# Performance work log

Measured on AMD Instinct MI355X. Metric: run time of the kernel, lower is better.

Reference implementation:

```python
import jax, jax.numpy as jnp
import numpy as np

N_NODES = 100000
N_EDGES = 1000000
NUM_FEATURES = 64
HIDDEN = 64
NUM_GRAPHS = 128


def setup_inputs() -> dict:
    key = jax.random.key(0)
    ks = jax.random.split(key, 12)
    x = jax.random.normal(ks[0], (N_NODES, NUM_FEATURES), dtype=jnp.float32)
    edge_index = jax.random.randint(ks[1], (2, N_EDGES), 0, N_NODES, dtype=jnp.int64)
    edge_weight = jax.random.uniform(ks[2], (N_EDGES,), dtype=jnp.float32)
    batch = jnp.sort(jax.random.randint(ks[3], (N_NODES,), 0, NUM_GRAPHS, dtype=jnp.int64))
    s1 = 1.0 / np.sqrt(NUM_FEATURES)
    s2 = 1.0 / np.sqrt(HIDDEN)
    # GraphConv layer 1: lin_rel (with bias) applied to aggregated msgs, lin_root (no bias)
    w1_rel = jax.random.uniform(ks[4], (HIDDEN, NUM_FEATURES), jnp.float32, -s1, s1)
    b1_rel = jax.random.uniform(ks[5], (HIDDEN,), jnp.float32, -s1, s1)
    w1_root = jax.random.uniform(ks[6], (HIDDEN, NUM_FEATURES), jnp.float32, -s1, s1)
    # GraphConv layer 2
    w2_rel = jax.random.uniform(ks[7], (HIDDEN, HIDDEN), jnp.float32, -s2, s2)
    b2_rel = jax.random.uniform(ks[8], (HIDDEN,), jnp.float32, -s2, s2)
    w2_root = jax.random.uniform(ks[9], (HIDDEN, HIDDEN), jnp.float32, -s2, s2)
    # final Linear(hidden, 1)
    w_lin = jax.random.uniform(ks[10], (1, HIDDEN), jnp.float32, -s2, s2)
    b_lin = jax.random.uniform(ks[11], (1,), jnp.float32, -s2, s2)
    return {
        "x": x, "edge_index": edge_index, "edge_weight": edge_weight, "batch": batch,
        "w1_rel": w1_rel, "b1_rel": b1_rel, "w1_root": w1_root,
        "w2_rel": w2_rel, "b2_rel": b2_rel, "w2_root": w2_root,
        "w_lin": w_lin, "b_lin": b_lin,
    }


def graph_conv(x, edge_index, edge_weight, w_rel, b_rel, w_root):
    # messages: x[src] * e, scatter-add into dst  (gather-scale-scatter)
    src, dst = edge_index[0], edge_index[1]
    msgs = x[src] * edge_weight[:, None]                      # [E, F]
    aggr = jax.ops.segment_sum(msgs, dst, num_segments=x.shape[0])  # [N, F]
    return aggr @ w_rel.T + b_rel + x @ w_root.T


def reference(x, edge_index, edge_weight, batch,
              w1_rel, b1_rel, w1_root, w2_rel, b2_rel, w2_root, w_lin, b_lin):
    h = graph_conv(x, edge_index, edge_weight, w1_rel, b1_rel, w1_root)
    h = jax.nn.relu(h)
    h = graph_conv(h, edge_index, edge_weight, w2_rel, b2_rel, w2_root)
    # global_mean_pool over graph ids
    sums = jax.ops.segment_sum(h, batch, num_segments=NUM_GRAPHS)          # [G, H]
    counts = jax.ops.segment_sum(jnp.ones((h.shape[0],), h.dtype), batch,
                                 num_segments=NUM_GRAPHS)                  # [G]
    pooled = sums / jnp.maximum(counts, 1.0)[:, None]
    # dropout(p=0.5) in eval mode is identity
    return pooled @ w_lin.T + b_lin                                        # [G, 1]
```

## Files before the change

### kernel.cpp

```cpp
#include <hip/hip_runtime.h>
#include <hip/hip_bf16.h>


#define N_NODES 100000
#define N_EDGES 1000000
#define NGRAPHS 128
#define BN 512
#define NBUCK ((N_NODES + BN - 1) / BN)
#define FILL_T 16
#define FILL_TILE (256 * FILL_T)
#define FILL_NB ((N_EDGES + FILL_TILE - 1) / FILL_TILE)
#define NTILES (N_NODES / 16)
#define AST 72

#define PREP_CVT_NB 3125
#define HIST0 (PREP_CVT_NB + 1)
#define HIST_NB 256
#define CNT0 (HIST0 + HIST_NB)
#define CNT_NB 64
#define PREP_TOTAL (CNT0 + CNT_NB)

typedef __attribute__((ext_vector_type(8))) short bf16x8;
typedef __attribute__((ext_vector_type(8))) unsigned short u16x8;
typedef __attribute__((ext_vector_type(4))) float f32x4;
typedef __attribute__((ext_vector_type(2))) float f32x2;

__device__ __forceinline__ unsigned short f2bf(float f) {
    unsigned u = __float_as_uint(f);
    unsigned r = (u + 0x7FFFu + ((u >> 16) & 1u)) >> 16;
    return (unsigned short)r;
}
__device__ __forceinline__ float bf2f(unsigned short h) {
    return __uint_as_float(((unsigned)h) << 16);
}
__device__ __forceinline__ void fma4(int w, float wt, float* a) {
    f32x2 lo = __builtin_amdgcn_cvt_pk_f32_fp8(w, false);
    f32x2 hi = __builtin_amdgcn_cvt_pk_f32_fp8(w, true);
    a[0] += wt * lo[0];
    a[1] += wt * lo[1];
    a[2] += wt * hi[0];
    a[3] += wt * hi[1];
}
__device__ __forceinline__ int pack4(float f0, float f1, float f2, float f3) {
    int w = __builtin_amdgcn_cvt_pk_fp8_f32(f0, f1, 0, false);
    w = __builtin_amdgcn_cvt_pk_fp8_f32(f2, f3, w, true);
    return w;
}

__global__ __launch_bounds__(256) void prep_all_kernel(
    const float* __restrict__ x, unsigned short* __restrict__ xh,
    int* __restrict__ xf8,
    const float* __restrict__ w1rel, const float* __restrict__ w1root,
    const float* __restrict__ w2rel, const float* __restrict__ w2root,
    const float* __restrict__ wlin, const float* __restrict__ b2rel,
    const float* __restrict__ blin, unsigned short* __restrict__ whirel,
    unsigned short* __restrict__ wlorel, unsigned short* __restrict__ whiroot,
    unsigned short* __restrict__ wloroot, float* __restrict__ u,
    float* __restrict__ v, float* __restrict__ C,
    const int* __restrict__ ei, int* __restrict__ bcount,
    const int* __restrict__ batch, float* __restrict__ gc, int E) {
    int tid = threadIdx.x;
    if (blockIdx.x < PREP_CVT_NB) {
        int i = blockIdx.x * 256 + tid;
        const float4* xp = (const float4*)x + (size_t)i * 2;
        float4 a = xp[0], b = xp[1];
        u16x8 o;
        o[0] = f2bf(a.x); o[1] = f2bf(a.y); o[2] = f2bf(a.z); o[3] = f2bf(a.w);
        o[4] = f2bf(b.x); o[5] = f2bf(b.y); o[6] = f2bf(b.z); o[7] = f2bf(b.w);
        *((u16x8*)xh + i) = o;
        int2 o8;
        o8.x = pack4(a.x, a.y, a.z, a.w);
        o8.y = pack4(b.x, b.y, b.z, b.w);
        *((int2*)xf8 + i) = o8;
        return;
    }
    if (blockIdx.x == PREP_CVT_NB) {
        for (int k = tid; k < 4096; k += 256) {
            float a = w1rel[k];
            unsigned short hi = f2bf(a);
            whirel[k] = hi;
            wlorel[k] = f2bf(a - bf2f(hi));
            float b = w1root[k];
            unsigned short hb = f2bf(b);
            whiroot[k] = hb;
            wloroot[k] = f2bf(b - bf2f(hb));
        }
        if (tid < 64) {
            float uu = 0.f, vv = 0.f;
            for (int h = 0; h < 64; ++h) {
                float wl = wlin[h];
                uu += wl * w2rel[h * 64 + tid];
                vv += wl * w2root[h * 64 + tid];
            }
            u[tid] = uu;
            v[tid] = vv;
        }
        if (tid == 0) {
            float c = blin[0];
            for (int h = 0; h < 64; ++h) c += wlin[h] * b2rel[h];
            *C = c;
        }
        return;
    }
    if (blockIdx.x < CNT0) {
        __shared__ int lh[NBUCK];
        for (int i = tid; i < NBUCK; i += 256) lh[i] = 0;
        __syncthreads();
        int bid2 = blockIdx.x - HIST0;
        for (int e = bid2 * 256 + tid; e < E; e += HIST_NB * 256)
            atomicAdd(&lh[ei[E + e] >> 9], 1);
        __syncthreads();
        for (int i = tid; i < NBUCK; i += 256) {
            int c = lh[i];
            if (c) atomicAdd(&bcount[i], c);
        }
        return;
    }
    {
        __shared__ int lgc[NGRAPHS];
        for (int i = tid; i < NGRAPHS; i += 256) lgc[i] = 0;
        __syncthreads();
        int bid2 = blockIdx.x - CNT0;
        for (int i = bid2 * 256 + tid; i < N_NODES; i += CNT_NB * 256)
            atomicAdd(&lgc[batch[i]], 1);
        __syncthreads();
        for (int i = tid; i < NGRAPHS; i += 256) {
            int c = lgc[i];
            if (c) atomicAdd(&gc[i], (float)c);
        }
    }
}

__global__ __launch_bounds__(256) void bucket_fill(
    const int* __restrict__ ei, const float* __restrict__ ew,
    const int* __restrict__ bcount, int* __restrict__ cursor,
    int2* __restrict__ ebuf, int E) {
    __shared__ int lh[NBUCK];
    __shared__ int gbase[NBUCK];
    __shared__ int sc[256];
    __shared__ int lbo[NBUCK];
    int tid = threadIdx.x;
    for (int i = tid; i < NBUCK; i += 256) lh[i] = 0;
    int v = (tid < NBUCK) ? bcount[tid] : 0;
    sc[tid] = v;
    __syncthreads();
    for (int off = 1; off < 256; off <<= 1) {
        int x = (tid >= off) ? sc[tid - off] : 0;
        __syncthreads();
        sc[tid] += x;
        __syncthreads();
    }
    if (tid < NBUCK) lbo[tid] = sc[tid] - v;
    __syncthreads();
    int base = blockIdx.x * FILL_TILE;
    int2 rec[FILL_T];
    int meta[FILL_T];
#pragma unroll
    for (int i = 0; i < FILL_T; ++i) {
        int e = base + i * 256 + tid;
        meta[i] = -1;
        if (e < E) {
            int src = ei[e];
            int dst = ei[E + e];
            int b = dst >> 9;
            int r = atomicAdd(&lh[b], 1);
            rec[i].x = src | ((dst & (BN - 1)) << 17);
            rec[i].y = __float_as_int(ew[e]);
            meta[i] = (b << 13) | r;
        }
    }
    __syncthreads();
    for (int i = tid; i < NBUCK; i += 256) {
        int c = lh[i];
        gbase[i] = c ? (lbo[i] + atomicAdd(&cursor[i], c)) : 0;
    }
    __syncthreads();
#pragma unroll
    for (int i = 0; i < FILL_T; ++i) {
        if (meta[i] >= 0) {
            int b = meta[i] >> 13;
            int r = meta[i] & 8191;
            ebuf[gbase[b] + r] = rec[i];
        }
    }
}

__global__ __launch_bounds__(512) void csr_build(
    const int* __restrict__ bcount, const int2* __restrict__ ebuf,
    const int* __restrict__ batch, int* __restrict__ row_ptr,
    int2* __restrict__ csr, int N) {
    __shared__ int s[BN];
    int b = blockIdx.x;
    int t = threadIdx.x;
    int vv = (t < NBUCK) ? bcount[t] : 0;
    if (t < 256) s[t] = vv;
    __syncthreads();
    for (int off = 1; off < 256; off <<= 1) {
        int x = (t >= off && t < 256) ? s[t - off] : 0;
        __syncthreads();
        if (t < 256) s[t] += x;
        __syncthreads();
    }
    int beg = (b == 0) ? 0 : s[b - 1];
    int end = s[b];
    __syncthreads();
    s[t] = 0;
    __syncthreads();
    for (int j = beg + t; j < end; j += 512)
        atomicAdd(&s[(ebuf[j].x >> 17) & (BN - 1)], 1);
    __syncthreads();
    int v = s[t];
    for (int off = 1; off < BN; off <<= 1) {
        int x = (t >= off) ? s[t - off] : 0;
        __syncthreads();
        s[t] += x;
        __syncthreads();
    }
    int excl = s[t] - v;
    int gidx = b * BN + t;
    if (gidx <= N) row_ptr[gidx] = beg + excl;
    __syncthreads();
    s[t] = excl;
    __syncthreads();
    for (int j = beg + t; j < end; j += 512) {
        int2 rec = ebuf[j];
        int dlo = (rec.x >> 17) & (BN - 1);
        int g = batch[b * BN + dlo];
        int r = atomicAdd(&s[dlo], 1);
        int2 o;
        o.x = (rec.x & 0x1FFFF) | (g << 17);
        o.y = rec.y;
        csr[beg + r] = o;
    }
}

__global__ __launch_bounds__(256) void gather_dense_kernel(
    const unsigned char* __restrict__ xf8, const unsigned short* __restrict__ xh,
    const int* __restrict__ row_ptr, const int2* __restrict__ csr,
    const unsigned short* __restrict__ whirel,
    const unsigned short* __restrict__ wlorel,
    const unsigned short* __restrict__ whiroot,
    const unsigned short* __restrict__ wloroot,
    const float* __restrict__ b1rel, const float* __restrict__ u,
    const float* __restrict__ v, float* __restrict__ p, float* __restrict__ q,
    int ntiles) {
    __shared__ unsigned short arow[4][16 * AST];
    int lane = threadIdx.x & 63;
    int wv = threadIdx.x >> 6;
    int wave = (blockIdx.x << 2) + wv;
    if (wave >= ntiles) return;
    unsigned short* my = &arow[wv][0];
    int nb = wave * 16;

    {
        int g4 = lane >> 2;
        int c4 = lane & 3;
        int node = nb + g4;
        int beg = row_ptr[node], end = row_ptr[node + 1];
        float a[16];
#pragma unroll
        for (int t = 0; t < 16; ++t) a[t] = 0.f;
        const unsigned char* xb = xf8 + (size_t)c4 * 16;
        for (int j = beg; j < end; j += 4) {
            int i1 = (j + 1 < end) ? j + 1 : j;
            int i2 = (j + 2 < end) ? j + 2 : j;
            int i3 = (j + 3 < end) ? j + 3 : j;
            int2 e0 = csr[j];
            int2 e1 = csr[i1];
            int2 e2 = csr[i2];
            int2 e3 = csr[i3];
            int4 r0 = *(const int4*)(xb + (size_t)(e0.x & 0x1FFFF) * 64);
            int4 r1 = *(const int4*)(xb + (size_t)(e1.x & 0x1FFFF) * 64);
            int4 r2 = *(const int4*)(xb + (size_t)(e2.x & 0x1FFFF) * 64);
            int4 r3 = *(const int4*)(xb + (size_t)(e3.x & 0x1FFFF) * 64);
            float w0 = __int_as_float(e0.y);
            float w1 = (j + 1 < end) ? __int_as_float(e1.y) : 0.f;
            float w2 = (j + 2 < end) ? __int_as_float(e2.y) : 0.f;
            float w3 = (j + 3 < end) ? __int_as_float(e3.y) : 0.f;
            fma4(r0.x, w0, a + 0);
            fma4(r0.y, w0, a + 4);
            fma4(r0.z, w0, a + 8);
            fma4(r0.w, w0, a + 12);
            fma4(r1.x, w1, a + 0);
            fma4(r1.y, w1, a + 4);
            fma4(r1.z, w1, a + 8);
            fma4(r1.w, w1, a + 12);
            fma4(r2.x, w2, a + 0);
            fma4(r2.y, w2, a + 4);
            fma4(r2.z, w2, a + 8);
            fma4(r2.w, w2, a + 12);
            fma4(r3.x, w3, a + 0);
            fma4(r3.y, w3, a + 4);
            fma4(r3.z, w3, a + 8);
            fma4(r3.w, w3, a + 12);
        }
        u16x8 o0, o1;
#pragma unroll
        for (int t = 0; t < 8; ++t) {
            o0[t] = f2bf(a[t]);
            o1[t] = f2bf(a[8 + t]);
        }
        *(u16x8*)(my + g4 * AST + c4 * 16) = o0;
        *(u16x8*)(my + g4 * AST + c4 * 16 + 8) = o1;
    }

    int lo4 = lane & 15;
    int quad = lane >> 4;
    f32x4 acc4[4];
#pragma unroll
    for (int t = 0; t < 4; ++t) acc4[t] = (f32x4){0.f, 0.f, 0.f, 0.f};
#pragma unroll
    for (int s = 0; s < 2; ++s) {
        bf16x8 Aa = *(const bf16x8*)(my + lo4 * AST + s * 32 + quad * 8);
        bf16x8 Ax = *(const bf16x8*)(xh + (size_t)(nb + lo4) * 64 + s * 32 +
                                     quad * 8);
#pragma unroll
        for (int t = 0; t < 4; ++t) {
            int off = (t * 16 + lo4) * 64 + s * 32 + quad * 8;
            bf16x8 bhr = *(const bf16x8*)(whirel + off);
            bf16x8 blr = *(const bf16x8*)(wlorel + off);
            bf16x8 bhx = *(const bf16x8*)(whiroot + off);
            bf16x8 blx = *(const bf16x8*)(wloroot + off);
            acc4[t] = __builtin_amdgcn_mfma_f32_16x16x32_bf16(Aa, bhr, acc4[t],
                                                              0, 0, 0);
            acc4[t] = __builtin_amdgcn_mfma_f32_16x16x32_bf16(Aa, blr, acc4[t],
                                                              0, 0, 0);
            acc4[t] = __builtin_amdgcn_mfma_f32_16x16x32_bf16(Ax, bhx, acc4[t],
                                                              0, 0, 0);
            acc4[t] = __builtin_amdgcn_mfma_f32_16x16x32_bf16(Ax, blx, acc4[t],
                                                              0, 0, 0);
        }
    }

    float pc[4] = {0.f, 0.f, 0.f, 0.f};
    float qc[4] = {0.f, 0.f, 0.f, 0.f};
#pragma unroll
    for (int t = 0; t < 4; ++t) {
        float bb = b1rel[t * 16 + lo4];
        float uu = u[t * 16 + lo4];
        float vv = v[t * 16 + lo4];
#pragma unroll
        for (int r = 0; r < 4; ++r) {
            float h1 = fmaxf(acc4[t][r] + bb, 0.f);
            pc[r] += uu * h1;
            qc[r] += vv * h1;
        }
    }
#pragma unroll
    for (int off = 1; off < 16; off <<= 1) {
#pragma unroll
        for (int r = 0; r < 4; ++r) {
            pc[r] += __shfl_xor(pc[r], off);
            qc[r] += __shfl_xor(qc[r], off);
        }
    }
    if (lo4 == 0) {
        f32x4 po = {pc[0], pc[1], pc[2], pc[3]};
        f32x4 qo = {qc[0], qc[1], qc[2], qc[3]};
        *(f32x4*)(p + nb + quad * 4) = po;
        *(f32x4*)(q + nb + quad * 4) = qo;
    }
}

#define PT_EPT 8
#define PT_EPW (64 * PT_EPT)
#define PT_NB ((N_EDGES + 4 * PT_EPW - 1) / (4 * PT_EPW))
#define PS_NB 98
__global__ __launch_bounds__(256) void pool_both(
    const int2* __restrict__ csr, const float* __restrict__ p,
    const float* __restrict__ q, const int* __restrict__ batch,
    float* __restrict__ gp, float* __restrict__ gq,
    const float* __restrict__ gc, int* __restrict__ done,
    const float* __restrict__ C, float* __restrict__ out, int E, int N) {
    __shared__ float lbuf[NGRAPHS];
    __shared__ int amLast;
    int tid = threadIdx.x;
    if (tid < NGRAPHS) lbuf[tid] = 0.f;
    __syncthreads();
    if (blockIdx.x < PT_NB) {
        int lane = tid & 63;
        int wid = (blockIdx.x * 256 + tid) >> 6;
        int base = wid * PT_EPW;
        float acc = 0.f;
        int curg = -1;
#pragma unroll
        for (int i = 0; i < PT_EPT; ++i) {
            int j = base + i * 64 + lane;
            if (j < E) {
                int2 e = csr[j];
                int g = ((unsigned)e.x) >> 17;
                float val = __int_as_float(e.y) * p[e.x & 0x1FFFF];
                if (g != curg) {
                    if (curg >= 0) atomicAdd(&lbuf[curg], acc);
                    curg = g;
                    acc = 0.f;
                }
                acc += val;
            }
        }
        if (curg >= 0) atomicAdd(&lbuf[curg], acc);
        __syncthreads();
        if (tid < NGRAPHS) {
            float t = lbuf[tid];
            if (t != 0.f) atomicAdd(&gp[tid], t);
        }
    } else {
        int bid = blockIdx.x - PT_NB;
        for (int i = bid * 256 + tid; i < N; i += PS_NB * 256) {
            atomicAdd(&lbuf[batch[i]], q[i]);
        }
        __syncthreads();
        if (tid < NGRAPHS) {
            float t = lbuf[tid];
            if (t != 0.f) atomicAdd(&gq[tid], t);
        }
    }
    __syncthreads();
    if (tid == 0) {
        __threadfence();
        amLast = (atomicAdd(done, 1) == PT_NB + PS_NB - 1);
    }
    __syncthreads();
    if (amLast) {
        __threadfence();
        if (tid < NGRAPHS) {
            float pv = atomicAdd(&gp[tid], 0.f);
            float qv = atomicAdd(&gq[tid], 0.f);
            float cv = atomicAdd((float*)&gc[tid], 0.f);
            out[tid] = (pv + qv) / fmaxf(cv, 1.f) + C[0];
        }
    }
}

extern "C" void kernel_launch(void* const* d_in, const int* in_sizes, int n_in,
                              void* d_out, int out_size, void* d_ws,
                              size_t ws_size, hipStream_t stream) {
    const float* x      = (const float*)d_in[0];
    const int*   ei     = (const int*)d_in[1];
    const float* ew     = (const float*)d_in[2];
    const int*   batch  = (const int*)d_in[3];
    const float* w1rel  = (const float*)d_in[4];
    const float* b1rel  = (const float*)d_in[5];
    const float* w1root = (const float*)d_in[6];
    const float* w2rel  = (const float*)d_in[7];
    const float* b2rel  = (const float*)d_in[8];
    const float* w2root = (const float*)d_in[9];
    const float* wlin   = (const float*)d_in[10];
    const float* blin   = (const float*)d_in[11];
    float* out = (float*)d_out;

    char* wsb = (char*)d_ws;
    int2* csr  = (int2*)wsb;
    int2* ebuf = (int2*)(wsb + (size_t)N_EDGES * 8);
    char* tail = wsb + (size_t)N_EDGES * 16;
    unsigned short* whirel  = (unsigned short*)tail;
    unsigned short* wlorel  = whirel + 4096;
    unsigned short* whiroot = wlorel + 4096;
    unsigned short* wloroot = whiroot + 4096;
    float* p  = (float*)(wloroot + 4096);
    float* q  = p + N_NODES;
    float* u  = q + N_NODES;
    float* v  = u + 64;
    float* C  = v + 64;
    int*   bcount = (int*)(C + 1);
    float* gp = (float*)(bcount + NBUCK);
    float* gq = gp + NGRAPHS;
    float* gc = gq + NGRAPHS;
    int*   done   = (int*)(gc + NGRAPHS);
    int*   cursor = done + 1;
    int*   row_ptr = cursor + NBUCK;
    unsigned short* xh = (unsigned short*)(row_ptr + N_NODES + 2);
    int*   xf8 = (int*)(xh + (size_t)N_NODES * 64);

    hipMemsetAsync(bcount, 0, (2 * NBUCK + 3 * NGRAPHS + 1) * sizeof(int),
                   stream);

    prep_all_kernel<<<PREP_TOTAL, 256, 0, stream>>>(
        x, xh, xf8, w1rel, w1root, w2rel, w2root, wlin, b2rel, blin, whirel,
        wlorel, whiroot, wloroot, u, v, C, ei, bcount, batch, gc, N_EDGES);

    bucket_fill<<<FILL_NB, 256, 0, stream>>>(ei, ew, bcount, cursor, ebuf,
                                             N_EDGES);
    csr_build<<<NBUCK, 512, 0, stream>>>(bcount, ebuf, batch, row_ptr, csr,
                                         N_NODES);

    gather_dense_kernel<<<(NTILES + 3) / 4, 256, 0, stream>>>(
        (const unsigned char*)xf8, xh, row_ptr, csr, whirel, wlorel, whiroot,
        wloroot, b1rel, u, v, p, q, NTILES);

    pool_both<<<PT_NB + PS_NB, 256, 0, stream>>>(csr, p, q, batch, gp, gq, gc,
                                                 done, C, out, N_EDGES,
                                                 N_NODES);
}
```

Measured before the change: 209.0 us.

## Build CSR via per-node degree histogram and global atomic cursor fill

```diff
diff --git a/kernel.cpp b/kernel.cpp
--- a/kernel.cpp
+++ b/kernel.cpp
@@ -7,9 +7,6 @@
 #define NGRAPHS 128
 #define BN 512
 #define NBUCK ((N_NODES + BN - 1) / BN)
-#define FILL_T 16
-#define FILL_TILE (256 * FILL_T)
-#define FILL_NB ((N_EDGES + FILL_TILE - 1) / FILL_TILE)
 #define NTILES (N_NODES / 16)
 #define AST 72
 
@@ -19,6 +16,8 @@
 #define CNT0 (HIST0 + HIST_NB)
 #define CNT_NB 64
 #define PREP_TOTAL (CNT0 + CNT_NB)
+
+#define FILL2_NB 977
 
 typedef __attribute__((ext_vector_type(8))) short bf16x8;
 typedef __attribute__((ext_vector_type(8))) unsigned short u16x8;
@@ -57,8 +56,9 @@
     unsigned short* __restrict__ wlorel, unsigned short* __restrict__ whiroot,
     unsigned short* __restrict__ wloroot, float* __restrict__ u,
     float* __restrict__ v, float* __restrict__ C,
-    const int* __restrict__ ei, int* __restrict__ bcount,
-    const int* __restrict__ batch, float* __restrict__ gc, int E) {
+    const int* __restrict__ ei, int* __restrict__ degree,
+    int* __restrict__ bcount, const int* __restrict__ batch,
+    float* __restrict__ gc, int E) {
     int tid = threadIdx.x;
     if (blockIdx.x < PREP_CVT_NB) {
         int i = blockIdx.x * 256 + tid;
@@ -106,9 +106,12 @@
         __shared__ int lh[NBUCK];
         for (int i = tid; i < NBUCK; i += 256) lh[i] = 0;
         __syncthreads();
-        int bid2 = blockIdx.x - HIST0;
-        for (int e = bid2 * 256 + tid; e < E; e += HIST_NB * 256)
-            atomicAdd(&lh[ei[E + e] >> 9], 1);
+        int hb = blockIdx.x - HIST0;
+        for (int e = hb * 256 + tid; e < E; e += HIST_NB * 256) {
+            int dst = ei[E + e];
+            atomicAdd(&degree[dst], 1);
+            atomicAdd(&lh[dst >> 9], 1);
+        }
         __syncthreads();
         for (int i = tid; i < NBUCK; i += 256) {
             int c = lh[i];
@@ -120,8 +123,8 @@
         __shared__ int lgc[NGRAPHS];
         for (int i = tid; i < NGRAPHS; i += 256) lgc[i] = 0;
         __syncthreads();
-        int bid2 = blockIdx.x - CNT0;
-        for (int i = bid2 * 256 + tid; i < N_NODES; i += CNT_NB * 256)
+        int cb = blockIdx.x - CNT0;
+        for (int i = cb * 256 + tid; i < N_NODES; i += CNT_NB * 256)
             atomicAdd(&lgc[batch[i]], 1);
         __syncthreads();
         for (int i = tid; i < NGRAPHS; i += 256) {
@@ -131,106 +134,57 @@
     }
 }
 
-__global__ __launch_bounds__(256) void bucket_fill(
-    const int* __restrict__ ei, const float* __restrict__ ew,
-    const int* __restrict__ bcount, int* __restrict__ cursor,
-    int2* __restrict__ ebuf, int E) {
-    __shared__ int lh[NBUCK];
-    __shared__ int gbase[NBUCK];
-    __shared__ int sc[256];
-    __shared__ int lbo[NBUCK];
-    int tid = threadIdx.x;
-    for (int i = tid; i < NBUCK; i += 256) lh[i] = 0;
-    int v = (tid < NBUCK) ? bcount[tid] : 0;
-    sc[tid] = v;
+__global__ __launch_bounds__(512) void scan_kernel(
+    const int* __restrict__ bcount, const int* __restrict__ degree,
+    int* __restrict__ row_ptr, int* __restrict__ cursor, int N, int E) {
+    __shared__ int sb[BN];
+    __shared__ int sc196[256];
+    int t = threadIdx.x;
+    int b = blockIdx.x;
+    if (t < 256) sc196[t] = (t < NBUCK) ? bcount[t] : 0;
     __syncthreads();
     for (int off = 1; off < 256; off <<= 1) {
-        int x = (tid >= off) ? sc[tid - off] : 0;
-        __syncthreads();
-        sc[tid] += x;
-        __syncthreads();
-    }
-    if (tid < NBUCK) lbo[tid] = sc[tid] - v;
+        int xv = 0;
+        if (t < 256 && t >= off) xv = sc196[t - off];
+        __syncthreads();
+        if (t < 256) sc196[t] += xv;
+        __syncthreads();
+    }
+    int beg = (b == 0) ? 0 : sc196[b - 1];
+    int gidx = b * BN + t;
+    int d = (gidx < N) ? degree[gidx] : 0;
+    sb[t] = d;
     __syncthreads();
-    int base = blockIdx.x * FILL_TILE;
-    int2 rec[FILL_T];
-    int meta[FILL_T];
-#pragma unroll
-    for (int i = 0; i < FILL_T; ++i) {
-        int e = base + i * 256 + tid;
-        meta[i] = -1;
+    for (int off = 1; off < BN; off <<= 1) {
+        int xv = (t >= off) ? sb[t - off] : 0;
+        __syncthreads();
+        sb[t] += xv;
+        __syncthreads();
+    }
+    int rp = beg + sb[t] - d;
+    if (gidx <= N) row_ptr[gidx] = rp;
+    if (gidx < N) cursor[gidx] = rp;
+}
+
+__global__ __launch_bounds__(256) void fill_kernel(
+    const int* __restrict__ ei, const float* __restrict__ ew,
+    const int* __restrict__ batch, int* __restrict__ cursor,
+    int2* __restrict__ csr, int E) {
+    int tid = threadIdx.x;
+#pragma unroll
+    for (int i = 0; i < 4; ++i) {
+        int e = blockIdx.x * 1024 + i * 256 + tid;
         if (e < E) {
             int src = ei[e];
             int dst = ei[E + e];
-            int b = dst >> 9;
-            int r = atomicAdd(&lh[b], 1);
-            rec[i].x = src | ((dst & (BN - 1)) << 17);
-            rec[i].y = __float_as_int(ew[e]);
-            meta[i] = (b << 13) | r;
-        }
-    }
-    __syncthreads();
-    for (int i = tid; i < NBUCK; i += 256) {
-        int c = lh[i];
-        gbase[i] = c ? (lbo[i] + atomicAdd(&cursor[i], c)) : 0;
-    }
-    __syncthreads();
-#pragma unroll
-    for (int i = 0; i < FILL_T; ++i) {
-        if (meta[i] >= 0) {
-            int b = meta[i] >> 13;
-            int r = meta[i] & 8191;
-            ebuf[gbase[b] + r] = rec[i];
-        }
-    }
-}
-
-__global__ __launch_bounds__(512) void csr_build(
-    const int* __restrict__ bcount, const int2* __restrict__ ebuf,
-    const int* __restrict__ batch, int* __restrict__ row_ptr,
-    int2* __restrict__ csr, int N) {
-    __shared__ int s[BN];
-    int b = blockIdx.x;
-    int t = threadIdx.x;
-    int vv = (t < NBUCK) ? bcount[t] : 0;
-    if (t < 256) s[t] = vv;
-    __syncthreads();
-    for (int off = 1; off < 256; off <<= 1) {
-        int x = (t >= off && t < 256) ? s[t - off] : 0;
-        __syncthreads();
-        if (t < 256) s[t] += x;
-        __syncthreads();
-    }
-    int beg = (b == 0) ? 0 : s[b - 1];
-    int end = s[b];
-    __syncthreads();
-    s[t] = 0;
-    __syncthreads();
-    for (int j = beg + t; j < end; j += 512)
-        atomicAdd(&s[(ebuf[j].x >> 17) & (BN - 1)], 1);
-    __syncthreads();
-    int v = s[t];
-    for (int off = 1; off < BN; off <<= 1) {
-        int x = (t >= off) ? s[t - off] : 0;
-        __syncthreads();
-        s[t] += x;
-        __syncthreads();
-    }
-    int excl = s[t] - v;
-    int gidx = b * BN + t;
-    if (gidx <= N) row_ptr[gidx] = beg + excl;
-    __syncthreads();
-    s[t] = excl;
-    __syncthreads();
-    for (int j = beg + t; j < end; j += 512) {
-        int2 rec = ebuf[j];
-        int dlo = (rec.x >> 17) & (BN - 1);
-        int g = batch[b * BN + dlo];
-        int r = atomicAdd(&s[dlo], 1);
-        int2 o;
-        o.x = (rec.x & 0x1FFFF) | (g << 17);
-        o.y = rec.y;
-        csr[beg + r] = o;
+            float w = ew[e];
+            int g = batch[dst];
+            int r = atomicAdd(&cursor[dst], 1);
+            int2 o;
+            o.x = src | (g << 17);
+            o.y = __float_as_int(w);
+            csr[r] = o;
+        }
     }
 }
 
@@ -251,7 +205,6 @@
     if (wave >= ntiles) return;
     unsigned short* my = &arow[wv][0];
     int nb = wave * 16;
-
     {
         int g4 = lane >> 2;
         int c4 = lane & 3;
@@ -303,7 +256,6 @@
         *(u16x8*)(my + g4 * AST + c4 * 16) = o0;
         *(u16x8*)(my + g4 * AST + c4 * 16 + 8) = o1;
     }
-
     int lo4 = lane & 15;
     int quad = lane >> 4;
     f32x4 acc4[4];
@@ -331,7 +283,6 @@
                                                               0, 0, 0);
         }
     }
-
     float pc[4] = {0.f, 0.f, 0.f, 0.f};
     float qc[4] = {0.f, 0.f, 0.f, 0.f};
 #pragma unroll
@@ -450,39 +401,41 @@
     float* out = (float*)d_out;
 
     char* wsb = (char*)d_ws;
-    int2* csr  = (int2*)wsb;
-    int2* ebuf = (int2*)(wsb + (size_t)N_EDGES * 8);
+    int2* csr = (int2*)wsb;
+    int* degree = (int*)(wsb + (size_t)N_EDGES * 8);
+    int* bcount = degree + N_NODES;
+    float* gp = (float*)(bcount + NBUCK);
+    float* gq = gp + NGRAPHS;
+    float* gc = gq + NGRAPHS;
+    int* done = (int*)(gc + NGRAPHS);
+    int* cursor = done + 1;
+    int* row_ptr = cursor + N_NODES;
     char* tail = wsb + (size_t)N_EDGES * 16;
     unsigned short* whirel  = (unsigned short*)tail;
     unsigned short* wlorel  = whirel + 4096;
     unsigned short* whiroot = wlorel + 4096;
     unsigned short* wloroot = whiroot + 4096;
-    float* p  = (float*)(wloroot + 4096);
-    float* q  = p + N_NODES;
-    float* u  = q + N_NODES;
-    float* v  = u + 64;
-    float* C  = v + 64;
-    int*   bcount = (int*)(C + 1);
-    float* gp = (float*)(bcount + NBUCK);
-    float* gq = gp + NGRAPHS;
-    float* gc = gq + NGRAPHS;
-    int*   done   = (int*)(gc + NGRAPHS);
-    int*   cursor = done + 1;
-    int*   row_ptr = cursor + NBUCK;
-    unsigned short* xh = (unsigned short*)(row_ptr + N_NODES + 2);
-    int*   xf8 = (int*)(xh + (size_t)N_NODES * 64);
-
-    hipMemsetAsync(bcount, 0, (2 * NBUCK + 3 * NGRAPHS + 1) * sizeof(int),
-                   stream);
+    float* p = (float*)(wloroot + 4096);
+    float* q = p + N_NODES;
+    float* u = q + N_NODES;
+    float* v = u + 64;
+    float* C = v + 64;
+    unsigned short* xh = (unsigned short*)(C + 1);
+    int* xf8 = (int*)(xh + (size_t)N_NODES * 64);
+
+    hipMemsetAsync(degree, 0,
+                   (N_NODES + NBUCK + 3 * NGRAPHS + 1) * sizeof(int), stream);
 
     prep_all_kernel<<<PREP_TOTAL, 256, 0, stream>>>(
         x, xh, xf8, w1rel, w1root, w2rel, w2root, wlin, b2rel, blin, whirel,
-        wlorel, whiroot, wloroot, u, v, C, ei, bcount, batch, gc, N_EDGES);
-
-    bucket_fill<<<FILL_NB, 256, 0, stream>>>(ei, ew, bcount, cursor, ebuf,
-                                             N_EDGES);
-    csr_build<<<NBUCK, 512, 0, stream>>>(bcount, ebuf, batch, row_ptr, csr,
-                                         N_NODES);
+        wlorel, whiroot, wloroot, u, v, C, ei, degree, bcount, batch, gc,
+        N_EDGES);
+
+    scan_kernel<<<NBUCK, 512, 0, stream>>>(bcount, degree, row_ptr, cursor,
+                                           N_NODES, N_EDGES);
+
+    fill_kernel<<<FILL2_NB, 256, 0, stream>>>(ei, ew, batch, cursor, csr,
+                                              N_EDGES);
 
     gather_dense_kernel<<<(NTILES + 3) / 4, 256, 0, stream>>>(
         (const unsigned char*)xf8, xh, row_ptr, csr, whirel, wlorel, whiroot,
```

Measured after the change: 274.5 us. 1.31x slower.
